# Kernel tuning notes

Hardware: AMD Instinct MI355X
Metric: run time of the kernel (lower is better)

The kernel has to match this reference:

```python
import jax, jax.numpy as jnp
import numpy as np

B, H, W, C = 4, 192, 640, 32
S = 32
STEPS = np.arange(S, dtype=np.float32)  # depth steps (init kwarg 'steps')


def setup_inputs() -> dict:
    key = jax.random.key(0)
    k1, k2, k3, k4, k5 = jax.random.split(key, 5)
    x = jax.random.normal(k1, (B, H, W, C), jnp.float32)
    y = jax.random.normal(k2, (B, H, W, C), jnp.float32)
    # principal point near image center, focal ~500px, small translation T12
    origin = jnp.array([[W / 2.0, H / 2.0]], jnp.float32) + jax.random.uniform(k3, (B, 2), jnp.float32)
    focal = 500.0 + 50.0 * jax.random.uniform(k4, (B, 2), jnp.float32)
    T12 = 0.01 * jax.random.normal(k5, (B, 3), jnp.float32)
    return {"x": x, "y": y, "origin": origin, "focal": focal, "T12": T12}


def _bilinear_1img(img, sx, sy):
    # img [H,W,C]; sx [W]: source x-coord for each output column; sy [H]: source y per row.
    # Matches tf.contrib.image.transform BILINEAR with fill value 0 outside the image.
    x0 = jnp.floor(sx); fx = sx - x0
    y0 = jnp.floor(sy); fy = sy - y0
    x0i = x0.astype(jnp.int32); x1i = x0i + 1
    y0i = y0.astype(jnp.int32); y1i = y0i + 1
    mx0 = ((x0i >= 0) & (x0i < W)).astype(img.dtype)
    mx1 = ((x1i >= 0) & (x1i < W)).astype(img.dtype)
    my0 = ((y0i >= 0) & (y0i < H)).astype(img.dtype)
    my1 = ((y1i >= 0) & (y1i < H)).astype(img.dtype)
    # interpolate along y first (transform is separable: x'=a*x+b, y'=a*y+c)
    r0 = img[jnp.clip(y0i, 0, H - 1)]                     # [H,W,C]
    r1 = img[jnp.clip(y1i, 0, H - 1)]                     # [H,W,C]
    rows = (my0 * (1.0 - fy))[:, None, None] * r0 + (my1 * fy)[:, None, None] * r1
    c0 = rows[:, jnp.clip(x0i, 0, W - 1)]                 # [H,W,C]
    c1 = rows[:, jnp.clip(x1i, 0, W - 1)]
    return (mx0 * (1.0 - fx))[None, :, None] * c0 + (mx1 * fx)[None, :, None] * c1


_warp = jax.vmap(lambda img, a, b, c: _bilinear_1img(
    img,
    a * jnp.arange(W, dtype=img.dtype) + b,
    a * jnp.arange(H, dtype=img.dtype) + c))


def reference(x, y, origin, focal, T12):
    tz = T12[:, 2]  # [B]

    def per_step(d):
        safe_d = jnp.where(d == 0.0, 1.0, d)
        D = jnp.where(d == 0.0, 0.0, 1.0 / (1.0 / safe_d + tz))          # [B]
        alpha = 1.0 - D * tz                                              # [B]
        beta = D * tz * origin[:, 0] + D * focal[:, 0] * T12[:, 0]        # [B]
        gamma = D * tz * origin[:, 1] + D * focal[:, 1] * T12[:, 1]       # [B]
        shifted = _warp(x, alpha, beta, gamma)                            # [B,H,W,C]
        return jnp.mean(shifted * y, axis=3)                              # [B,H,W]

    corr = jax.lax.map(jax.checkpoint(per_step), jnp.asarray(STEPS))      # [S,B,H,W]
    return jnp.transpose(corr, (1, 2, 3, 0))                              # [B,H,W,S]
```

## Files before the change

### kernel.cpp

```cpp
#include <hip/hip_runtime.h>
#include <hip/hip_fp16.h>

#define BB 4
#define HH 192
#define WW 640
#define CC 32
#define SS 32
#define PXB 64
#define MAXW 140
#define PLANE (MAXW + 1)

typedef _Float16 half2n __attribute__((ext_vector_type(2)));

#if defined(__has_builtin)
#if __has_builtin(__builtin_amdgcn_fdot2)
#define HAS_FDOT2 1
#endif
#endif

static __device__ __forceinline__ float fdot2_acc(__half2 a, __half2 b, float acc) {
#ifdef HAS_FDOT2
    return __builtin_amdgcn_fdot2(__builtin_bit_cast(half2n, a),
                                  __builtin_bit_cast(half2n, b), acc, false);
#else
    const float2 af = __half22float2(a);
    const float2 bf = __half22float2(b);
    return acc + af.x * bf.x + af.y * bf.y;
#endif
}

static __device__ __forceinline__ unsigned pk2(float w) {
    return (unsigned)__builtin_bit_cast(unsigned short, __float2half_rn(w)) * 0x10001u;
}

__global__ __launch_bounds__(256) void convert_x_kernel(const float* __restrict__ x,
                                                        __half* __restrict__ xh) {
    const size_t i = ((size_t)blockIdx.x * 256 + threadIdx.x) * 8;
    const float4 f0 = *(const float4*)(x + i);
    const float4 f1 = *(const float4*)(x + i + 4);
    uint4 u;
    u.x = __builtin_bit_cast(unsigned, __floats2half2_rn(f0.x, f0.y));
    u.y = __builtin_bit_cast(unsigned, __floats2half2_rn(f0.z, f0.w));
    u.z = __builtin_bit_cast(unsigned, __floats2half2_rn(f1.x, f1.y));
    u.w = __builtin_bit_cast(unsigned, __floats2half2_rn(f1.z, f1.w));
    *(uint4*)(xh + i) = u;
}

__global__ __launch_bounds__(64, 4) void corr_kernel(
    const __half* __restrict__ xh, const float* __restrict__ y,
    const float* __restrict__ origin, const float* __restrict__ focal,
    const float* __restrict__ T12, float* __restrict__ out)
{
    __shared__ uint4 sU[SS];
    __shared__ uint4 sV[SS];
    __shared__ uint4 comb[4][PLANE];

    const int lane = threadIdx.x;

    const int p0 = blockIdx.x * PXB;
    const int w0 = p0 % WW;
    const int h  = (p0 / WW) % HH;
    const int b  = p0 / (WW * HH);

    if (lane < SS) {
        const float tz = T12[b * 3 + 2];
        const float kx = tz * origin[b * 2 + 0] + focal[b * 2 + 0] * T12[b * 3 + 0];
        const float ky = tz * origin[b * 2 + 1] + focal[b * 2 + 1] * T12[b * 3 + 1];
        const float sf = (float)lane;
        const float D = sf * __builtin_amdgcn_rcpf(1.0f + sf * tz);
        const float alpha = 1.0f - D * tz;
        const float dkx = D * kx;
        const float dky = D * ky;

        const float syv = alpha * (float)h + dky;
        const float y0f = floorf(syv);
        const float fy  = syv - y0f;
        const int   y0  = (int)y0f;
        const int   y1  = y0 + 1;
        const float wy0 = (y0 >= 0 && y0 < HH) ? (1.0f - fy) : 0.0f;
        const float wy1 = (y1 >= 0 && y1 < HH) ? fy : 0.0f;
        const int   cy0 = min(max(y0, 0), HH - 1);
        const int   cy1 = min(max(y1, 0), HH - 1);

        const float sxa = alpha * (float)w0 + dkx;
        const float sxb = alpha * (float)(w0 + PXB - 1) + dkx;
        const int xlo = (int)floorf(fminf(sxa, sxb));
        const int xhi = (int)floorf(fmaxf(sxa, sxb)) + 1;
        const int width4 = (xhi - xlo + 1) * 4;

        uint4 U, V;
        U.x = __builtin_bit_cast(unsigned, alpha);
        U.y = __builtin_bit_cast(unsigned, dkx);
        U.z = (unsigned)xlo;
        U.w = (unsigned)width4;
        V.x = (unsigned)((cy0 * WW) << 6);
        V.y = (unsigned)((cy1 * WW) << 6);
        V.z = pk2(wy0);
        V.w = pk2(wy1);
        sU[lane] = U;
        sV[lane] = V;
    }

    const int pme = p0 + lane;
    __half2 yh[16];
    {
        const float4* yp = (const float4*)(y + (size_t)pme * CC);
#pragma unroll
        for (int q = 0; q < 8; ++q) {
            const float4 f = yp[q];
            yh[2 * q]     = __floats2half2_rn(f.x, f.y);
            yh[2 * q + 1] = __floats2half2_rn(f.z, f.w);
        }
    }

    const char* xbase = (const char*)(xh + (size_t)b * HH * WW * CC);
    const float pxf = (float)(w0 + lane);
    float* outp = out + (size_t)pme * SS;

    __syncthreads();

#pragma unroll 1
    for (int g = 0; g < 4; ++g) {
        float res[8];
#pragma unroll
        for (int j = 0; j < 8; ++j) {
            const int s = g * 8 + j;
            const uint4 U = sU[s];
            const uint4 V = sV[s];
            const float alpha  = __builtin_bit_cast(float, U.x);
            const float dkx    = __builtin_bit_cast(float, U.y);
            const int   xlo    = (int)U.z;
            const int   width4 = (int)U.w;
            const bool  fits   = (width4 <= MAXW * 4);

            const float sx  = alpha * pxf + dkx;
            const float x0f = floorf(sx);
            const float fx  = sx - x0f;
            const int   x0  = (int)x0f;
            const int   x1  = x0 + 1;
            const float wx0f = (x0 >= 0 && x0 < WW) ? (1.0f - fx) : 0.0f;
            const float wx1f = (x1 >= 0 && x1 < WW) ? fx : 0.0f;
            const __half2 wx0 = __builtin_bit_cast(__half2, pk2(wx0f));
            const __half2 wx1 = __builtin_bit_cast(__half2, pk2(wx1f));
            const int cx0 = min(max(x0, 0), WW - 1);
            const int cx1 = min(max(x1, 0), WW - 1);

            if (fits) {
                const __half2 wy0h = __builtin_bit_cast(__half2, V.z);
                const __half2 wy1h = __builtin_bit_cast(__half2, V.w);
                for (int c = lane; c < width4; c += 64) {
                    const int cpx = min(max(xlo + (c >> 2), 0), WW - 1);
                    const unsigned po = (unsigned)((cpx << 6) + ((c & 3) << 4));
                    const uint4 a  = *(const uint4*)(xbase + (size_t)(V.x + po));
                    const uint4 bq = *(const uint4*)(xbase + (size_t)(V.y + po));
                    uint4 o;
#pragma unroll
                    for (int i = 0; i < 4; ++i) {
                        __half2 r = __hmul2(__builtin_bit_cast(__half2, (&a.x)[i]), wy0h);
                        r = __hfma2(__builtin_bit_cast(__half2, (&bq.x)[i]), wy1h, r);
                        (&o.x)[i] = __builtin_bit_cast(unsigned, r);
                    }
                    comb[c & 3][c >> 2] = o;
                }
            }
            __syncthreads();

            float acc = 0.0f;
            if (fits) {
                const int wlim = (width4 >> 2) - 1;
                const int l0 = min(max(cx0 - xlo, 0), wlim);
                const int l1 = min(max(cx1 - xlo, 0), wlim);
                const uint4* b0 = &comb[0][l0];
                const uint4* b1 = &comb[0][l1];
                uint4 A[4], Bq[4];
#pragma unroll
                for (int i = 0; i < 4; ++i) {
                    A[i]  = b0[i * PLANE];
                    Bq[i] = b1[i * PLANE];
                }
#pragma unroll
                for (int i = 0; i < 4; ++i) {
#pragma unroll
                    for (int w = 0; w < 4; ++w) {
                        __half2 v = __hmul2(__builtin_bit_cast(__half2, (&A[i].x)[w]), wx0);
                        v = __hfma2(__builtin_bit_cast(__half2, (&Bq[i].x)[w]), wx1, v);
                        acc = fdot2_acc(v, yh[i * 4 + w], acc);
                    }
                }
            } else {
                const __half2 wy0h = __builtin_bit_cast(__half2, V.z);
                const __half2 wy1h = __builtin_bit_cast(__half2, V.w);
                const uint4* r0p0 = (const uint4*)(xbase + (size_t)(V.x + ((unsigned)cx0 << 6)));
                const uint4* r0p1 = (const uint4*)(xbase + (size_t)(V.x + ((unsigned)cx1 << 6)));
                const uint4* r1p0 = (const uint4*)(xbase + (size_t)(V.y + ((unsigned)cx0 << 6)));
                const uint4* r1p1 = (const uint4*)(xbase + (size_t)(V.y + ((unsigned)cx1 << 6)));
#pragma unroll
                for (int i = 0; i < 4; ++i) {
                    const uint4 a  = r0p0[i];
                    const uint4 bq = r0p1[i];
                    const uint4 c2 = r1p0[i];
                    const uint4 d  = r1p1[i];
#pragma unroll
                    for (int w = 0; w < 4; ++w) {
                        __half2 top = __hmul2(__builtin_bit_cast(__half2, (&a.x)[w]), wx0);
                        top = __hfma2(__builtin_bit_cast(__half2, (&bq.x)[w]), wx1, top);
                        __half2 bot = __hmul2(__builtin_bit_cast(__half2, (&c2.x)[w]), wx0);
                        bot = __hfma2(__builtin_bit_cast(__half2, (&d.x)[w]), wx1, bot);
                        __half2 v = __hmul2(top, wy0h);
                        v = __hfma2(bot, wy1h, v);
                        acc = fdot2_acc(v, yh[i * 4 + w], acc);
                    }
                }
            }
            __syncthreads();

            res[j] = acc * (1.0f / 32.0f);
        }
        *(float4*)(outp + g * 8)     = make_float4(res[0], res[1], res[2], res[3]);
        *(float4*)(outp + g * 8 + 4) = make_float4(res[4], res[5], res[6], res[7]);
    }
}

extern "C" void kernel_launch(void* const* d_in, const int* in_sizes, int n_in,
                              void* d_out, int out_size, void* d_ws, size_t ws_size,
                              hipStream_t stream) {
    const float* x = (const float*)d_in[0];
    const float* y = (const float*)d_in[1];
    const float* origin = (const float*)d_in[2];
    const float* focal = (const float*)d_in[3];
    const float* T12 = (const float*)d_in[4];
    float* out = (float*)d_out;
    __half* xh = (__half*)d_ws;

    const int nelem = BB * HH * WW * CC;
    convert_x_kernel<<<nelem / (256 * 8), 256, 0, stream>>>(x, xh);

    const int npix = BB * HH * WW;
    corr_kernel<<<npix / PXB, 64, 0, stream>>>(xh, y, origin, focal, T12, out);
}
```

Baseline: 336.9 us.

## Prefetch next depth step's rows into registers and swizzle block order across XCDs

The global loads and LDS fill for depth step s+1 are now issued before computing step s. When the row span fits in 5×64 slots, loads go into register arrays and are written to the shared combined buffer after the current dot products, so load latency overlaps compute. This removes one barrier per step, relying on the block being a single 64-lane wave. Block indices are also remapped so consecutive launched blocks are spread across eight groups, which changes cache locality per XCD. In exchange, register use rises and control flow gets more complex.

After: 324.5 us. 3.7% less time.

```diff
diff --git a/kernel.cpp b/kernel.cpp
--- a/kernel.cpp
+++ b/kernel.cpp
@@ -7,8 +7,10 @@
 #define CC 32
 #define SS 32
 #define PXB 64
+#define NWG (BB * HH * WW / PXB)
 #define MAXW 140
 #define PLANE (MAXW + 1)
+#define PW 5
 
 typedef _Float16 half2n __attribute__((ext_vector_type(2)));
 
@@ -56,8 +58,9 @@
     __shared__ uint4 comb[4][PLANE];
 
     const int lane = threadIdx.x;
-
-    const int p0 = blockIdx.x * PXB;
+    const int bid = ((int)blockIdx.x & 7) * (NWG >> 3) + ((int)blockIdx.x >> 3);
+
+    const int p0 = bid * PXB;
     const int w0 = p0 % WW;
     const int h  = (p0 / WW) % HH;
     const int b  = p0 / (WW * HH);
@@ -119,19 +122,42 @@
 
     __syncthreads();
 
+    uint4 U = sU[0];
+    uint4 V = sV[0];
+    {
+        const int xlo    = (int)U.z;
+        const int width4 = (int)U.w;
+        if (width4 <= MAXW * 4) {
+            const __half2 wy0h = __builtin_bit_cast(__half2, V.z);
+            const __half2 wy1h = __builtin_bit_cast(__half2, V.w);
+            for (int c = lane; c < width4; c += 64) {
+                const int cpx = min(max(xlo + (c >> 2), 0), WW - 1);
+                const unsigned po = (unsigned)((cpx << 6) + ((c & 3) << 4));
+                const uint4 a  = *(const uint4*)(xbase + (size_t)(V.x + po));
+                const uint4 bq = *(const uint4*)(xbase + (size_t)(V.y + po));
+                uint4 o;
+#pragma unroll
+                for (int i = 0; i < 4; ++i) {
+                    __half2 r = __hmul2(__builtin_bit_cast(__half2, (&a.x)[i]), wy0h);
+                    r = __hfma2(__builtin_bit_cast(__half2, (&bq.x)[i]), wy1h, r);
+                    (&o.x)[i] = __builtin_bit_cast(unsigned, r);
+                }
+                comb[c & 3][c >> 2] = o;
+            }
+            __syncthreads();
+        }
+    }
+
 #pragma unroll 1
     for (int g = 0; g < 4; ++g) {
         float res[8];
 #pragma unroll
         for (int j = 0; j < 8; ++j) {
             const int s = g * 8 + j;
-            const uint4 U = sU[s];
-            const uint4 V = sV[s];
             const float alpha  = __builtin_bit_cast(float, U.x);
             const float dkx    = __builtin_bit_cast(float, U.y);
             const int   xlo    = (int)U.z;
             const int   width4 = (int)U.w;
-            const bool  fits   = (width4 <= MAXW * 4);
 
             const float sx  = alpha * pxf + dkx;
             const float x0f = floorf(sx);
@@ -145,28 +171,30 @@
             const int cx0 = min(max(x0, 0), WW - 1);
             const int cx1 = min(max(x1, 0), WW - 1);
 
-            if (fits) {
-                const __half2 wy0h = __builtin_bit_cast(__half2, V.z);
-                const __half2 wy1h = __builtin_bit_cast(__half2, V.w);
-                for (int c = lane; c < width4; c += 64) {
-                    const int cpx = min(max(xlo + (c >> 2), 0), WW - 1);
-                    const unsigned po = (unsigned)((cpx << 6) + ((c & 3) << 4));
-                    const uint4 a  = *(const uint4*)(xbase + (size_t)(V.x + po));
-                    const uint4 bq = *(const uint4*)(xbase + (size_t)(V.y + po));
-                    uint4 o;
-#pragma unroll
-                    for (int i = 0; i < 4; ++i) {
-                        __half2 r = __hmul2(__builtin_bit_cast(__half2, (&a.x)[i]), wy0h);
-                        r = __hfma2(__builtin_bit_cast(__half2, (&bq.x)[i]), wy1h, r);
-                        (&o.x)[i] = __builtin_bit_cast(unsigned, r);
-                    }
-                    comb[c & 3][c >> 2] = o;
+            uint4 pa[PW], pb[PW];
+            uint4 Un, Vn;
+            int tn = 3, xlon = 0, width4n = 0;
+            if (s + 1 < SS) {
+                Un = sU[s + 1];
+                Vn = sV[s + 1];
+                xlon    = (int)Un.z;
+                width4n = (int)Un.w;
+                tn = (width4n <= PW * 64) ? 0 : ((width4n <= MAXW * 4) ? 1 : 2);
+                if (tn == 0) {
+#pragma unroll
+                    for (int i = 0; i < PW; ++i) {
+                        const int c  = lane + i * 64;
+                        const int cc = min(c, width4n - 1);
+                        const int cpx = min(max(xlon + (cc >> 2), 0), WW - 1);
+                        const unsigned po = (unsigned)((cpx << 6) + ((cc & 3) << 4));
+                        pa[i] = *(const uint4*)(xbase + (size_t)(Vn.x + po));
+                        pb[i] = *(const uint4*)(xbase + (size_t)(Vn.y + po));
+                    }
                 }
             }
-            __syncthreads();
 
             float acc = 0.0f;
-            if (fits) {
+            if (width4 <= MAXW * 4) {
                 const int wlim = (width4 >> 2) - 1;
                 const int l0 = min(max(cx0 - xlo, 0), wlim);
                 const int l1 = min(max(cx1 - xlo, 0), wlim);
@@ -212,7 +240,48 @@
                     }
                 }
             }
-            __syncthreads();
+
+            if (s + 1 < SS) {
+                if (tn == 0) {
+                    const __half2 wy0h = __builtin_bit_cast(__half2, Vn.z);
+                    const __half2 wy1h = __builtin_bit_cast(__half2, Vn.w);
+#pragma unroll
+                    for (int i = 0; i < PW; ++i) {
+                        const int c = lane + i * 64;
+                        if (c < width4n) {
+                            uint4 o;
+#pragma unroll
+                            for (int q = 0; q < 4; ++q) {
+                                __half2 r = __hmul2(__builtin_bit_cast(__half2, (&pa[i].x)[q]), wy0h);
+                                r = __hfma2(__builtin_bit_cast(__half2, (&pb[i].x)[q]), wy1h, r);
+                                (&o.x)[q] = __builtin_bit_cast(unsigned, r);
+                            }
+                            comb[c & 3][c >> 2] = o;
+                        }
+                    }
+                    __syncthreads();
+                } else if (tn == 1) {
+                    const __half2 wy0h = __builtin_bit_cast(__half2, Vn.z);
+                    const __half2 wy1h = __builtin_bit_cast(__half2, Vn.w);
+                    for (int c = lane; c < width4n; c += 64) {
+                        const int cpx = min(max(xlon + (c >> 2), 0), WW - 1);
+                        const unsigned po = (unsigned)((cpx << 6) + ((c & 3) << 4));
+                        const uint4 a  = *(const uint4*)(xbase + (size_t)(Vn.x + po));
+                        const uint4 bq = *(const uint4*)(xbase + (size_t)(Vn.y + po));
+                        uint4 o;
+#pragma unroll
+                        for (int q = 0; q < 4; ++q) {
+                            __half2 r = __hmul2(__builtin_bit_cast(__half2, (&a.x)[q]), wy0h);
+                            r = __hfma2(__builtin_bit_cast(__half2, (&bq.x)[q]), wy1h, r);
+                            (&o.x)[q] = __builtin_bit_cast(unsigned, r);
+                        }
+                        comb[c & 3][c >> 2] = o;
+                    }
+                    __syncthreads();
+                }
+                U = Un;
+                V = Vn;
+            }
 
             res[j] = acc * (1.0f / 32.0f);
         }
@@ -235,6 +304,5 @@
     const int nelem = BB * HH * WW * CC;
     convert_x_kernel<<<nelem / (256 * 8), 256, 0, stream>>>(x, xh);
 
-    const int npix = BB * HH * WW;
-    corr_kernel<<<npix / PXB, 64, 0, stream>>>(xh, y, origin, focal, T12, out);
-}
+    corr_kernel<<<NWG, 64, 0, stream>>>(xh, y, origin, focal, T12, out);
+}
```
